# Optimization experiments

Hardware: AMD Instinct MI355X
Metric: run time of the kernel (lower is better)

The kernel has to match this reference:

```python
import math
import jax, jax.numpy as jnp
import numpy as np

B, L, D = 64, 1024, 64

def setup_inputs() -> dict:
    key = jax.random.key(0)
    k1, k2, k3, k4, k5, k6 = jax.random.split(key, 6)
    return {
        "queries": jax.random.normal(k1, (B, L, D), dtype=jnp.float32),
        "keys": jax.random.normal(k2, (B, L, D), dtype=jnp.float32),
        "values": jax.random.normal(k3, (B, L, D), dtype=jnp.float32),
        "pos_k": jax.random.normal(k4, (L, L, D), dtype=jnp.float32),
        "pos_v": jax.random.normal(k5, (L, L, D), dtype=jnp.float32),
        "valid_lens": jax.random.randint(k6, (B,), 0, L, dtype=jnp.int32),
    }

MASK_VALUE = -1e6  # matches torch source's -1000000.0 fill

def reference(queries, keys, values, pos_k, pos_v, valid_lens):
    d = queries.shape[-1]
    scale = 1.0 / math.sqrt(d)
    # content scores: [B, Lq, Lk]
    scores = jnp.einsum("bqd,bkd->bqk", queries, keys)
    # relative-position scores: contract each query position with its RPR key table
    scores_pos = jnp.einsum("bqd,qkd->bqk", queries, pos_k)
    scores = (scores + scores_pos) * scale
    # mask keys beyond valid_lens[b] with -1e6 (as in sequence_mask), then softmax
    kpos = jnp.arange(scores.shape[-1])
    mask = kpos[None, None, :] < valid_lens[:, None, None]  # [B,1,Lk] -> broadcast
    scores = jnp.where(mask, scores, MASK_VALUE)
    attn = jax.nn.softmax(scores, axis=-1)  # [B, Lq, Lk]
    # dropout prob = 0.0 -> identity
    out = jnp.einsum("bqk,bkd->bqd", attn, values)
    out_pos = jnp.einsum("bqk,qkd->bqd", attn, pos_v)
    return out + out_pos
```

## Files before the change

kernel.cpp:

```cpp
#include <hip/hip_runtime.h>
#include <hip/hip_bf16.h>

typedef __attribute__((ext_vector_type(8))) short bf16x8;
typedef __attribute__((ext_vector_type(4))) float f32x4;

#define B_SZ 64
#define L_SZ 1024
#define D_SZ 64
#define SCALE 0.125f

__device__ __forceinline__ short f2bf(float f) {
    union { float f; unsigned u; } v; v.f = f;
    unsigned r = (v.u + 0x7fffu + ((v.u >> 16) & 1u)) >> 16;
    return (short)r;
}

__device__ __forceinline__ bf16x8 cvt8(const float* __restrict__ p) {
    f32x4 a = *(const f32x4*)p;
    f32x4 b = *(const f32x4*)(p + 4);
    bf16x8 r;
    r[0] = f2bf(a[0]); r[1] = f2bf(a[1]); r[2] = f2bf(a[2]); r[3] = f2bf(a[3]);
    r[4] = f2bf(b[0]); r[5] = f2bf(b[1]); r[6] = f2bf(b[2]); r[7] = f2bf(b[3]);
    return r;
}

#define MFMA(A, Bf, C) __builtin_amdgcn_mfma_f32_16x16x32_bf16(A, Bf, C, 0, 0, 0)

__global__ void cvt_bf16_k(const float* __restrict__ src, short* __restrict__ dst, int n8) {
    const int stride = gridDim.x * blockDim.x;
    for (int i = blockIdx.x * blockDim.x + threadIdx.x; i < n8; i += stride) {
        *(bf16x8*)(dst + (size_t)i * 8) = cvt8(src + (size_t)i * 8);
    }
}

#define TP 72
__global__ void tr64_bf16_k(const float* __restrict__ src, short* __restrict__ dst) {
    __shared__ __attribute__((aligned(16))) short tile[64 * TP];
    const int kt = blockIdx.x;
    const size_t o = blockIdx.y;
    const int tid = threadIdx.x;
    {
        const int rr = tid >> 2, c0 = (tid & 3) << 4;
        const float* sp = src + (o * L_SZ + (size_t)(kt * 64 + rr)) * D_SZ + c0;
        *(bf16x8*)(tile + rr * TP + c0)     = cvt8(sp);
        *(bf16x8*)(tile + rr * TP + c0 + 8) = cvt8(sp + 8);
    }
    __syncthreads();
    {
        const int d = tid >> 2, k4 = (tid & 3) << 4;
        bf16x8 o0, o1;
#pragma unroll
        for (int j = 0; j < 8; ++j) {
            o0[j] = tile[(k4 + j) * TP + d];
            o1[j] = tile[(k4 + 8 + j) * TP + d];
        }
        short* dp = dst + (o * 64 + (size_t)d) * L_SZ + kt * 64 + k4;
        *(bf16x8*)dp       = o0;
        *(bf16x8*)(dp + 8) = o1;
    }
}

__global__ __launch_bounds__(512, 2) void rpr_attn_bf16(
    const short* __restrict__ Qb, const short* __restrict__ Kb,
    const short* __restrict__ Vt, const short* __restrict__ PKb,
    const short* __restrict__ PVt, const int* __restrict__ VLEN,
    float* __restrict__ OUT)
{
    __shared__ __attribute__((aligned(16))) float SA[2][256 * 32];
    __shared__ __attribute__((aligned(16))) short PB[2][256 * 64];

    const int tid = threadIdx.x;
    const int wave = tid >> 6, lane = tid & 63;
    const int g = wave >> 2, r = wave & 3;
    const int lane15 = lane & 15, quad = lane >> 4;

    const int n = blockIdx.x;
    const int l = (n & 7) * 32 + (n >> 3);
    const int b0 = (l & 3) * 16;
    const int q0 = (l >> 2) * 16;

    char* sa = (char*)&SA[g][0];
    char* pb = (char*)&PB[g][0];

    bf16x8 qa[4][2], qp[4][2];
    int vl[4];
#pragma unroll
    for (int j = 0; j < 4; ++j) {
        const int bl = r * 4 + j;
        vl[j] = VLEN[b0 + bl];
        const short* pc = Qb + ((b0 + bl) * L_SZ + q0 + lane15) * D_SZ + quad * 8;
        qa[j][0] = *(const bf16x8*)pc;
        qa[j][1] = *(const bf16x8*)(pc + 32);
        const short* pp = Qb + ((b0 + lane15) * L_SZ + q0 + bl) * D_SZ + quad * 8;
        qp[j][0] = *(const bf16x8*)pp;
        qp[j][1] = *(const bf16x8*)(pp + 32);
    }

    f32x4 Oc[4][4], Op[4][4];
    float es[4][4];
#pragma unroll
    for (int j = 0; j < 4; ++j)
#pragma unroll
        for (int nt = 0; nt < 4; ++nt) {
            Oc[j][nt] = (f32x4){0.f, 0.f, 0.f, 0.f};
            Op[j][nt] = (f32x4){0.f, 0.f, 0.f, 0.f};
            es[j][nt] = 0.f;
        }

    for (int it = 0; it < 16; ++it) {
        const int kb = g * 512 + it * 32;

#pragma unroll
        for (int j = 0; j < 4; ++j) {
            const int ql = r * 4 + j;
#pragma unroll
            for (int c = 0; c < 2; ++c) {
                const short* bp = PKb + ((q0 + ql) * L_SZ + kb + c * 16 + lane15) * D_SZ + quad * 8;
                f32x4 acc = (f32x4){0.f, 0.f, 0.f, 0.f};
                acc = MFMA(qp[j][0], *(const bf16x8*)bp, acc);
                acc = MFMA(qp[j][1], *(const bf16x8*)(bp + 32), acc);
#pragma unroll
                for (int i = 0; i < 4; ++i) {
                    const int brow = quad * 4 + i;
                    const int off = (((brow * 16 + ql) * 32 + c * 16 + lane15) * 4)
                                    ^ (((brow ^ ql) & 7) << 4);
                    *(float*)(sa + off) = acc[i];
                }
            }
        }
        __syncthreads();

#pragma unroll
        for (int j = 0; j < 4; ++j) {
            const int bl = r * 4 + j;
#pragma unroll
            for (int c = 0; c < 2; ++c) {
                const short* bp = Kb + ((b0 + bl) * L_SZ + kb + c * 16 + lane15) * D_SZ + quad * 8;
                f32x4 acc = (f32x4){0.f, 0.f, 0.f, 0.f};
                acc = MFMA(qa[j][0], *(const bf16x8*)bp, acc);
                acc = MFMA(qa[j][1], *(const bf16x8*)(bp + 32), acc);
                const int kg = kb + c * 16 + lane15;
#pragma unroll
                for (int i = 0; i < 4; ++i) {
                    const int q = quad * 4 + i;
                    const int soff = (((bl * 16 + q) * 32 + c * 16 + lane15) * 4)
                                     ^ (((bl ^ q) & 7) << 4);
                    const float s = (acc[i] + *(const float*)(sa + soff)) * SCALE;
                    float e;
                    if (vl[j] == 0)       e = 1.0f;
                    else if (kg < vl[j])  e = __expf(s);
                    else                  e = 0.0f;
                    es[j][i] += e;
                    const int poff = (((bl * 16 + q) * 64 + c * 16 + lane15) * 2)
                                     ^ (((bl ^ q) & 7) << 4);
                    *(short*)(pb + poff) = f2bf(e);
                }
            }
        }
        __syncthreads();

#pragma unroll
        for (int j = 0; j < 4; ++j) {
            const int bl = r * 4 + j;
            const int aoff = (((bl * 16 + lane15) * 64) * 2 + quad * 16)
                             ^ (((bl ^ lane15) & 7) << 4);
            const bf16x8 af = *(const bf16x8*)(pb + aoff);
            const short* vb = Vt + ((b0 + bl) * 64 + lane15) * L_SZ + kb + quad * 8;
#pragma unroll
            for (int nt = 0; nt < 4; ++nt) {
                const bf16x8 bf = *(const bf16x8*)(vb + nt * 16 * L_SZ);
                Oc[j][nt] = MFMA(af, bf, Oc[j][nt]);
            }
        }
#pragma unroll
        for (int j = 0; j < 4; ++j) {
            const int ql = r * 4 + j;
            const int aoff = (((lane15 * 16 + ql) * 64) * 2 + quad * 16)
                             ^ (((lane15 ^ ql) & 7) << 4);
            const bf16x8 af = *(const bf16x8*)(pb + aoff);
            const short* vb = PVt + ((q0 + ql) * 64 + lane15) * L_SZ + kb + quad * 8;
#pragma unroll
            for (int nt = 0; nt < 4; ++nt) {
                const bf16x8 bf = *(const bf16x8*)(vb + nt * 16 * L_SZ);
                Op[j][nt] = MFMA(af, bf, Op[j][nt]);
            }
        }
        __syncthreads();
    }

    float* lball = (float*)&PB[0][0];
#pragma unroll
    for (int j = 0; j < 4; ++j)
#pragma unroll
        for (int i = 0; i < 4; ++i) {
            float s = es[j][i];
            s += __shfl_xor(s, 1);
            s += __shfl_xor(s, 2);
            s += __shfl_xor(s, 4);
            s += __shfl_xor(s, 8);
            if (lane15 == 0)
                lball[g * 256 + (r * 4 + j) * 16 + quad * 4 + i] = s;
        }

    float* Obuf = &SA[0][0];

    if (g == 0) {
#pragma unroll
        for (int j = 0; j < 4; ++j)
#pragma unroll
            for (int nt = 0; nt < 4; ++nt)
#pragma unroll
                for (int i = 0; i < 4; ++i)
                    Obuf[((r * 4 + j) * 16 + quad * 4 + i) * 64 + nt * 16 + lane15] = Oc[j][nt][i];
    }
    __syncthreads();
    if (g == 1) {
#pragma unroll
        for (int j = 0; j < 4; ++j)
#pragma unroll
            for (int nt = 0; nt < 4; ++nt)
#pragma unroll
                for (int i = 0; i < 4; ++i)
                    Obuf[((r * 4 + j) * 16 + quad * 4 + i) * 64 + nt * 16 + lane15] += Oc[j][nt][i];
    }
    __syncthreads();
    if (g == 0) {
#pragma unroll
        for (int j = 0; j < 4; ++j)
#pragma unroll
            for (int nt = 0; nt < 4; ++nt)
#pragma unroll
                for (int i = 0; i < 4; ++i)
                    Obuf[((quad * 4 + i) * 16 + r * 4 + j) * 64 + nt * 16 + lane15] += Op[j][nt][i];
    }
    __syncthreads();
    if (g == 1) {
#pragma unroll
        for (int j = 0; j < 4; ++j)
#pragma unroll
            for (int nt = 0; nt < 4; ++nt)
#pragma unroll
                for (int i = 0; i < 4; ++i)
                    Obuf[((quad * 4 + i) * 16 + r * 4 + j) * 64 + nt * 16 + lane15] += Op[j][nt][i];
    }
    __syncthreads();

    for (int idx = tid; idx < 4096; idx += 512) {
        const int d4 = idx & 15, ql2 = (idx >> 4) & 15, bl2 = idx >> 8;
        const float li = lball[bl2 * 16 + ql2] + lball[256 + bl2 * 16 + ql2];
        const float rl = 1.0f / li;
        f32x4 o = *(const f32x4*)&Obuf[(bl2 * 16 + ql2) * 64 + d4 * 4];
        o[0] *= rl; o[1] *= rl; o[2] *= rl; o[3] *= rl;
        *(f32x4*)&OUT[((b0 + bl2) * L_SZ + q0 + ql2) * D_SZ + d4 * 4] = o;
    }
}

#define KP 36
#define BPITCH 580
#define SA_SZ 9280

__global__ __launch_bounds__(512, 2) void rpr_attn(
    const float* __restrict__ Q, const float* __restrict__ Kt,
    const float* __restrict__ V, const float* __restrict__ PK,
    const float* __restrict__ PV, const int* __restrict__ VLEN,
    float* __restrict__ OUT)
{
    __shared__ float SA[2][SA_SZ];
    __shared__ float lbuf[2][256];

    const int tid = threadIdx.x;
    const int wave = tid >> 6, lane = tid & 63;
    const int g = wave >> 2, r = wave & 3;
    const int lane15 = lane & 15, quad = lane >> 4;
    const int b0 = blockIdx.x * 16;
    const int q0 = blockIdx.y * 16;

    float* sa = SA[g];

    bf16x8 qa[4][2], qp[4][2];
    int vl[4];
#pragma unroll
    for (int j = 0; j < 4; ++j) {
        const int bl = r * 4 + j;
        vl[j] = VLEN[b0 + bl];
        const float* pc = Q + ((b0 + bl) * L_SZ + q0 + lane15) * D_SZ + quad * 8;
        qa[j][0] = cvt8(pc); qa[j][1] = cvt8(pc + 32);
        const float* pp = Q + ((b0 + lane15) * L_SZ + q0 + bl) * D_SZ + quad * 8;
        qp[j][0] = cvt8(pp); qp[j][1] = cvt8(pp + 32);
    }

    f32x4 Oc[4][4], Op[4][4];
#pragma unroll
    for (int j = 0; j < 4; ++j)
#pragma unroll
        for (int nt = 0; nt < 4; ++nt) {
            Oc[j][nt] = (f32x4){0.f, 0.f, 0.f, 0.f};
            Op[j][nt] = (f32x4){0.f, 0.f, 0.f, 0.f};
        }
    float l_acc = 0.f;

    const int tg = r * 64 + lane;
    const int lb = tg >> 4, lq = tg & 15;

    for (int it = 0; it < 16; ++it) {
        const int kb = g * 512 + it * 32;

#pragma unroll
        for (int j = 0; j < 4; ++j) {
            const int ql = r * 4 + j;
#pragma unroll
            for (int c = 0; c < 2; ++c) {
                const float* bp = PK + ((q0 + ql) * L_SZ + kb + c * 16 + lane15) * D_SZ + quad * 8;
                f32x4 acc = (f32x4){0.f, 0.f, 0.f, 0.f};
                acc = MFMA(qp[j][0], cvt8(bp), acc);
                acc = MFMA(qp[j][1], cvt8(bp + 32), acc);
#pragma unroll
                for (int i = 0; i < 4; ++i)
                    sa[(quad * 4 + i) * BPITCH + ql * KP + c * 16 + lane15] = acc[i];
            }
        }
        __syncthreads();

#pragma unroll
        for (int j = 0; j < 4; ++j) {
            const int bl = r * 4 + j;
#pragma unroll
            for (int c = 0; c < 2; ++c) {
                const float* bp = Kt + ((b0 + bl) * L_SZ + kb + c * 16 + lane15) * D_SZ + quad * 8;
                f32x4 acc = (f32x4){0.f, 0.f, 0.f, 0.f};
                acc = MFMA(qa[j][0], cvt8(bp), acc);
                acc = MFMA(qa[j][1], cvt8(bp + 32), acc);
                const int kg = kb + c * 16 + lane15;
#pragma unroll
                for (int i = 0; i < 4; ++i) {
                    const int idx = bl * BPITCH + (quad * 4 + i) * KP + c * 16 + lane15;
                    const float s = (acc[i] + sa[idx]) * SCALE;
                    float e;
                    if (vl[j] == 0)       e = 1.0f;
                    else if (kg < vl[j])  e = __expf(s);
                    else                  e = 0.0f;
                    sa[idx] = e;
                }
            }
        }
        __syncthreads();

        {
            const float* row = sa + lb * BPITCH + lq * KP;
            float s = 0.f;
#pragma unroll
            for (int kk = 0; kk < 32; kk += 4) {
                f32x4 v4 = *(const f32x4*)(row + kk);
                s += v4[0] + v4[1] + v4[2] + v4[3];
            }
            l_acc += s;
        }
#pragma unroll
        for (int j = 0; j < 4; ++j) {
            const int bl = r * 4 + j;
            const bf16x8 af = cvt8(sa + bl * BPITCH + lane15 * KP + quad * 8);
            const float* vb = V + ((b0 + bl) * L_SZ + kb + quad * 8) * D_SZ + lane15;
#pragma unroll
            for (int nt = 0; nt < 4; ++nt) {
                bf16x8 bf;
#pragma unroll
                for (int jj = 0; jj < 8; ++jj) bf[jj] = f2bf(vb[jj * D_SZ + nt * 16]);
                Oc[j][nt] = MFMA(af, bf, Oc[j][nt]);
            }
        }
#pragma unroll
        for (int j = 0; j < 4; ++j) {
            const int ql = r * 4 + j;
            const bf16x8 af = cvt8(sa + lane15 * BPITCH + ql * KP + quad * 8);
            const float* vb = PV + ((q0 + ql) * L_SZ + kb + quad * 8) * D_SZ + lane15;
#pragma unroll
            for (int nt = 0; nt < 4; ++nt) {
                bf16x8 bf;
#pragma unroll
                for (int jj = 0; jj < 8; ++jj) bf[jj] = f2bf(vb[jj * D_SZ + nt * 16]);
                Op[j][nt] = MFMA(af, bf, Op[j][nt]);
            }
        }
        __syncthreads();
    }

    lbuf[g][tg] = l_acc;
    float* Obuf = &SA[0][0];

    if (g == 0) {
#pragma unroll
        for (int j = 0; j < 4; ++j)
#pragma unroll
            for (int nt = 0; nt < 4; ++nt)
#pragma unroll
                for (int i = 0; i < 4; ++i)
                    Obuf[((r * 4 + j) * 16 + quad * 4 + i) * 64 + nt * 16 + lane15] = Oc[j][nt][i];
    }
    __syncthreads();
    if (g == 1) {
#pragma unroll
        for (int j = 0; j < 4; ++j)
#pragma unroll
            for (int nt = 0; nt < 4; ++nt)
#pragma unroll
                for (int i = 0; i < 4; ++i)
                    Obuf[((r * 4 + j) * 16 + quad * 4 + i) * 64 + nt * 16 + lane15] += Oc[j][nt][i];
    }
    __syncthreads();
    if (g == 0) {
#pragma unroll
        for (int j = 0; j < 4; ++j)
#pragma unroll
            for (int nt = 0; nt < 4; ++nt)
#pragma unroll
                for (int i = 0; i < 4; ++i)
                    Obuf[((quad * 4 + i) * 16 + r * 4 + j) * 64 + nt * 16 + lane15] += Op[j][nt][i];
    }
    __syncthreads();
    if (g == 1) {
#pragma unroll
        for (int j = 0; j < 4; ++j)
#pragma unroll
            for (int nt = 0; nt < 4; ++nt)
#pragma unroll
                for (int i = 0; i < 4; ++i)
                    Obuf[((quad * 4 + i) * 16 + r * 4 + j) * 64 + nt * 16 + lane15] += Op[j][nt][i];
    }
    __syncthreads();

    for (int idx = tid; idx < 4096; idx += 512) {
        const int d4 = idx & 15, ql2 = (idx >> 4) & 15, bl2 = idx >> 8;
        const float li = lbuf[0][bl2 * 16 + ql2] + lbuf[1][bl2 * 16 + ql2];
        const float rl = 1.0f / li;
        f32x4 o = *(const f32x4*)&Obuf[(bl2 * 16 + ql2) * 64 + d4 * 4];
        o[0] *= rl; o[1] *= rl; o[2] *= rl; o[3] *= rl;
        *(f32x4*)&OUT[((b0 + bl2) * L_SZ + q0 + ql2) * D_SZ + d4 * 4] = o;
    }
}

extern "C" void kernel_launch(void* const* d_in, const int* in_sizes, int n_in,
                              void* d_out, int out_size, void* d_ws, size_t ws_size,
                              hipStream_t stream) {
    (void)in_sizes; (void)n_in; (void)out_size;
    const float* Q  = (const float*)d_in[0];
    const float* K  = (const float*)d_in[1];
    const float* V  = (const float*)d_in[2];
    const float* PK = (const float*)d_in[3];
    const float* PV = (const float*)d_in[4];
    const int*   VL = (const int*)d_in[5];
    float* OUT = (float*)d_out;

    const size_t WS_NEEDED = (3ull * 4194304ull + 2ull * 67108864ull) * 2ull;

    if (d_ws != nullptr && ws_size >= WS_NEEDED) {
        short* Qb  = (short*)d_ws;
        short* Kb  = Qb + 4194304;
        short* Vt  = Kb + 4194304;
        short* PKb = Vt + 4194304;
        short* PVt = PKb + 67108864;

        cvt_bf16_k<<<dim3(1024), dim3(256), 0, stream>>>(Q, Qb, 524288);
        cvt_bf16_k<<<dim3(1024), dim3(256), 0, stream>>>(K, Kb, 524288);
        cvt_bf16_k<<<dim3(2048), dim3(256), 0, stream>>>(PK, PKb, 8388608);
        tr64_bf16_k<<<dim3(16, 64),   dim3(256), 0, stream>>>(V, Vt);
        tr64_bf16_k<<<dim3(16, 1024), dim3(256), 0, stream>>>(PV, PVt);

        rpr_attn_bf16<<<dim3(256), dim3(512), 0, stream>>>(Qb, Kb, Vt, PKb, PVt, VL, OUT);
    } else {
        dim3 grid(4, 64, 1);
        dim3 block(512, 1, 1);
        rpr_attn<<<grid, block, 0, stream>>>(Q, K, V, PK, PV, VL, OUT);
    }
}
```

Baseline: 1.259 ms.

## Drop bf16 pre-conversion of Q/K/PK, split key range across blocks with merge kernel

Removes the separate fp32→bf16 conversion kernels for Q, K and PK and converts them in registers inside the attention kernel. This avoids writing and re-reading a large bf16 copy of PK. The two key halves now run in separate 256-thread blocks that write partial outputs and row sums to workspace, and a new merge kernel combines them and normalizes. The change also adds s_setprio around the PV MFMA phase, drops a per-iteration barrier, and reworks the transpose kernel to stage fp32 in a padded tile. The cost is reading PK at fp32 width inside the main kernel plus an extra partial-output round trip through global memory.

```diff
diff --git a/kernel.cpp b/kernel.cpp
--- a/kernel.cpp
+++ b/kernel.cpp
@@ -4,7 +4,6 @@
 typedef __attribute__((ext_vector_type(8))) short bf16x8;
 typedef __attribute__((ext_vector_type(4))) float f32x4;
 
-#define B_SZ 64
 #define L_SZ 1024
 #define D_SZ 64
 #define SCALE 0.125f
@@ -26,24 +25,23 @@
 
 #define MFMA(A, Bf, C) __builtin_amdgcn_mfma_f32_16x16x32_bf16(A, Bf, C, 0, 0, 0)
 
-__global__ void cvt_bf16_k(const float* __restrict__ src, short* __restrict__ dst, int n8) {
-    const int stride = gridDim.x * blockDim.x;
-    for (int i = blockIdx.x * blockDim.x + threadIdx.x; i < n8; i += stride) {
-        *(bf16x8*)(dst + (size_t)i * 8) = cvt8(src + (size_t)i * 8);
-    }
-}
-
-#define TP 72
 __global__ void tr64_bf16_k(const float* __restrict__ src, short* __restrict__ dst) {
-    __shared__ __attribute__((aligned(16))) short tile[64 * TP];
+    __shared__ float tile[64 * 65];
     const int kt = blockIdx.x;
     const size_t o = blockIdx.y;
     const int tid = threadIdx.x;
     {
         const int rr = tid >> 2, c0 = (tid & 3) << 4;
         const float* sp = src + (o * L_SZ + (size_t)(kt * 64 + rr)) * D_SZ + c0;
-        *(bf16x8*)(tile + rr * TP + c0)     = cvt8(sp);
-        *(bf16x8*)(tile + rr * TP + c0 + 8) = cvt8(sp + 8);
+        f32x4 v0 = *(const f32x4*)sp;
+        f32x4 v1 = *(const f32x4*)(sp + 4);
+        f32x4 v2 = *(const f32x4*)(sp + 8);
+        f32x4 v3 = *(const f32x4*)(sp + 12);
+        float* tp = tile + rr * 65 + c0;
+        tp[0] = v0[0];  tp[1] = v0[1];  tp[2] = v0[2];  tp[3] = v0[3];
+        tp[4] = v1[0];  tp[5] = v1[1];  tp[6] = v1[2];  tp[7] = v1[3];
+        tp[8] = v2[0];  tp[9] = v2[1];  tp[10] = v2[2]; tp[11] = v2[3];
+        tp[12] = v3[0]; tp[13] = v3[1]; tp[14] = v3[2]; tp[15] = v3[3];
     }
     __syncthreads();
     {
@@ -51,8 +49,8 @@
         bf16x8 o0, o1;
 #pragma unroll
         for (int j = 0; j < 8; ++j) {
-            o0[j] = tile[(k4 + j) * TP + d];
-            o1[j] = tile[(k4 + 8 + j) * TP + d];
+            o0[j] = f2bf(tile[(k4 + j) * 65 + d]);
+            o1[j] = f2bf(tile[(k4 + 8 + j) * 65 + d]);
         }
         short* dp = dst + (o * 64 + (size_t)d) * L_SZ + kt * 64 + k4;
         *(bf16x8*)dp       = o0;
@@ -60,27 +58,27 @@
     }
 }
 
-__global__ __launch_bounds__(512, 2) void rpr_attn_bf16(
-    const short* __restrict__ Qb, const short* __restrict__ Kb,
-    const short* __restrict__ Vt, const short* __restrict__ PKb,
-    const short* __restrict__ PVt, const int* __restrict__ VLEN,
-    float* __restrict__ OUT)
+__global__ __launch_bounds__(256, 2) void rpr_attn2(
+    const float* __restrict__ Q, const float* __restrict__ K,
+    const float* __restrict__ PK,
+    const short* __restrict__ Vt, const short* __restrict__ PVt,
+    const int* __restrict__ VLEN,
+    float* __restrict__ Opart, float* __restrict__ Lp)
 {
-    __shared__ __attribute__((aligned(16))) float SA[2][256 * 32];
-    __shared__ __attribute__((aligned(16))) short PB[2][256 * 64];
+    __shared__ __attribute__((aligned(16))) float SH[16384 + 256];
+    char* sa = (char*)&SH[0];
+    char* pb = (char*)&SH[8192];
+    float* lbuf = &SH[16384];
 
     const int tid = threadIdx.x;
-    const int wave = tid >> 6, lane = tid & 63;
-    const int g = wave >> 2, r = wave & 3;
+    const int r = tid >> 6, lane = tid & 63;
     const int lane15 = lane & 15, quad = lane >> 4;
 
     const int n = blockIdx.x;
-    const int l = (n & 7) * 32 + (n >> 3);
+    const int l = (n & 7) * 64 + (n >> 3);
     const int b0 = (l & 3) * 16;
-    const int q0 = (l >> 2) * 16;
-
-    char* sa = (char*)&SA[g][0];
-    char* pb = (char*)&PB[g][0];
+    const int ks = (l >> 2) & 1;
+    const int q0 = (l >> 3) * 16;
 
     bf16x8 qa[4][2], qp[4][2];
     int vl[4];
@@ -88,12 +86,10 @@
     for (int j = 0; j < 4; ++j) {
         const int bl = r * 4 + j;
         vl[j] = VLEN[b0 + bl];
-        const short* pc = Qb + ((b0 + bl) * L_SZ + q0 + lane15) * D_SZ + quad * 8;
-        qa[j][0] = *(const bf16x8*)pc;
-        qa[j][1] = *(const bf16x8*)(pc + 32);
-        const short* pp = Qb + ((b0 + lane15) * L_SZ + q0 + bl) * D_SZ + quad * 8;
-        qp[j][0] = *(const bf16x8*)pp;
-        qp[j][1] = *(const bf16x8*)(pp + 32);
+        const float* pc = Q + ((b0 + bl) * L_SZ + q0 + lane15) * D_SZ + quad * 8;
+        qa[j][0] = cvt8(pc); qa[j][1] = cvt8(pc + 32);
+        const float* pp = Q + ((b0 + lane15) * L_SZ + q0 + bl) * D_SZ + quad * 8;
+        qp[j][0] = cvt8(pp); qp[j][1] = cvt8(pp + 32);
     }
 
     f32x4 Oc[4][4], Op[4][4];
@@ -108,17 +104,17 @@
         }
 
     for (int it = 0; it < 16; ++it) {
-        const int kb = g * 512 + it * 32;
+        const int kb = ks * 512 + it * 32;
 
 #pragma unroll
         for (int j = 0; j < 4; ++j) {
             const int ql = r * 4 + j;
 #pragma unroll
             for (int c = 0; c < 2; ++c) {
-                const short* bp = PKb + ((q0 + ql) * L_SZ + kb + c * 16 + lane15) * D_SZ + quad * 8;
+                const float* bp = PK + ((q0 + ql) * L_SZ + kb + c * 16 + lane15) * D_SZ + quad * 8;
                 f32x4 acc = (f32x4){0.f, 0.f, 0.f, 0.f};
-                acc = MFMA(qp[j][0], *(const bf16x8*)bp, acc);
-                acc = MFMA(qp[j][1], *(const bf16x8*)(bp + 32), acc);
+                acc = MFMA(qp[j][0], cvt8(bp), acc);
+                acc = MFMA(qp[j][1], cvt8(bp + 32), acc);
 #pragma unroll
                 for (int i = 0; i < 4; ++i) {
                     const int brow = quad * 4 + i;
@@ -135,10 +131,10 @@
             const int bl = r * 4 + j;
 #pragma unroll
             for (int c = 0; c < 2; ++c) {
-                const short* bp = Kb + ((b0 + bl) * L_SZ + kb + c * 16 + lane15) * D_SZ + quad * 8;
+                const float* bp = K + ((b0 + bl) * L_SZ + kb + c * 16 + lane15) * D_SZ + quad * 8;
                 f32x4 acc = (f32x4){0.f, 0.f, 0.f, 0.f};
-                acc = MFMA(qa[j][0], *(const bf16x8*)bp, acc);
-                acc = MFMA(qa[j][1], *(const bf16x8*)(bp + 32), acc);
+                acc = MFMA(qa[j][0], cvt8(bp), acc);
+                acc = MFMA(qa[j][1], cvt8(bp + 32), acc);
                 const int kg = kb + c * 16 + lane15;
 #pragma unroll
                 for (int i = 0; i < 4; ++i) {
@@ -159,6 +155,7 @@
         }
         __syncthreads();
 
+        __builtin_amdgcn_s_setprio(1);
 #pragma unroll
         for (int j = 0; j < 4; ++j) {
             const int bl = r * 4 + j;
@@ -185,10 +182,9 @@
                 Op[j][nt] = MFMA(af, bf, Op[j][nt]);
             }
         }
-        __syncthreads();
-    }
-
-    float* lball = (float*)&PB[0][0];
+        __builtin_amdgcn_s_setprio(0);
+    }
+
 #pragma unroll
     for (int j = 0; j < 4; ++j)
 #pragma unroll
@@ -199,59 +195,55 @@
             s += __shfl_xor(s, 4);
             s += __shfl_xor(s, 8);
             if (lane15 == 0)
-                lball[g * 256 + (r * 4 + j) * 16 + quad * 4 + i] = s;
-        }
-
-    float* Obuf = &SA[0][0];
-
-    if (g == 0) {
-#pragma unroll
-        for (int j = 0; j < 4; ++j)
-#pragma unroll
-            for (int nt = 0; nt < 4; ++nt)
-#pragma unroll
-                for (int i = 0; i < 4; ++i)
-                    Obuf[((r * 4 + j) * 16 + quad * 4 + i) * 64 + nt * 16 + lane15] = Oc[j][nt][i];
-    }
-    __syncthreads();
-    if (g == 1) {
-#pragma unroll
-        for (int j = 0; j < 4; ++j)
-#pragma unroll
-            for (int nt = 0; nt < 4; ++nt)
-#pragma unroll
-                for (int i = 0; i < 4; ++i)
-                    Obuf[((r * 4 + j) * 16 + quad * 4 + i) * 64 + nt * 16 + lane15] += Oc[j][nt][i];
-    }
-    __syncthreads();
-    if (g == 0) {
-#pragma unroll
-        for (int j = 0; j < 4; ++j)
-#pragma unroll
-            for (int nt = 0; nt < 4; ++nt)
-#pragma unroll
-                for (int i = 0; i < 4; ++i)
-                    Obuf[((quad * 4 + i) * 16 + r * 4 + j) * 64 + nt * 16 + lane15] += Op[j][nt][i];
-    }
-    __syncthreads();
-    if (g == 1) {
-#pragma unroll
-        for (int j = 0; j < 4; ++j)
-#pragma unroll
-            for (int nt = 0; nt < 4; ++nt)
-#pragma unroll
-                for (int i = 0; i < 4; ++i)
-                    Obuf[((quad * 4 + i) * 16 + r * 4 + j) * 64 + nt * 16 + lane15] += Op[j][nt][i];
-    }
-    __syncthreads();
-
-    for (int idx = tid; idx < 4096; idx += 512) {
+                lbuf[(r * 4 + j) * 16 + quad * 4 + i] = s;
+        }
+    __syncthreads();
+
+    float* Obuf = &SH[0];
+
+#pragma unroll
+    for (int j = 0; j < 4; ++j)
+#pragma unroll
+        for (int nt = 0; nt < 4; ++nt)
+#pragma unroll
+            for (int i = 0; i < 4; ++i)
+                Obuf[((r * 4 + j) * 16 + quad * 4 + i) * 64 + nt * 16 + lane15] = Oc[j][nt][i];
+    __syncthreads();
+#pragma unroll
+    for (int j = 0; j < 4; ++j)
+#pragma unroll
+        for (int nt = 0; nt < 4; ++nt)
+#pragma unroll
+            for (int i = 0; i < 4; ++i)
+                Obuf[((quad * 4 + i) * 16 + r * 4 + j) * 64 + nt * 16 + lane15] += Op[j][nt][i];
+    __syncthreads();
+
+    const size_t obase = (size_t)ks * 4194304;
+    for (int idx = tid; idx < 4096; idx += 256) {
         const int d4 = idx & 15, ql2 = (idx >> 4) & 15, bl2 = idx >> 8;
-        const float li = lball[bl2 * 16 + ql2] + lball[256 + bl2 * 16 + ql2];
-        const float rl = 1.0f / li;
         f32x4 o = *(const f32x4*)&Obuf[(bl2 * 16 + ql2) * 64 + d4 * 4];
-        o[0] *= rl; o[1] *= rl; o[2] *= rl; o[3] *= rl;
-        *(f32x4*)&OUT[((b0 + bl2) * L_SZ + q0 + ql2) * D_SZ + d4 * 4] = o;
+        *(f32x4*)&Opart[obase + (((size_t)(b0 + bl2) * L_SZ) + q0 + ql2) * D_SZ + d4 * 4] = o;
+    }
+    {
+        const int ql2 = tid & 15, bl2 = tid >> 4;
+        Lp[ks * 65536 + (b0 + bl2) * L_SZ + q0 + ql2] = lbuf[bl2 * 16 + ql2];
+    }
+}
+
+__global__ void merge_k(const float* __restrict__ Opart, const float* __restrict__ Lp,
+                        float* __restrict__ OUT) {
+    const int stride = gridDim.x * blockDim.x;
+    for (int u = blockIdx.x * blockDim.x + threadIdx.x; u < 1048576; u += stride) {
+        const int bq = u >> 4;
+        const float rl = 1.0f / (Lp[bq] + Lp[65536 + bq]);
+        f32x4 a = *(const f32x4*)(Opart + (size_t)u * 4);
+        f32x4 b = *(const f32x4*)(Opart + 4194304ull + (size_t)u * 4);
+        f32x4 o;
+        o[0] = (a[0] + b[0]) * rl;
+        o[1] = (a[1] + b[1]) * rl;
+        o[2] = (a[2] + b[2]) * rl;
+        o[3] = (a[3] + b[3]) * rl;
+        *(f32x4*)(OUT + (size_t)u * 4) = o;
     }
 }
 
@@ -450,22 +442,18 @@
     const int*   VL = (const int*)d_in[5];
     float* OUT = (float*)d_out;
 
-    const size_t WS_NEEDED = (3ull * 4194304ull + 2ull * 67108864ull) * 2ull;
+    const size_t WS_NEEDED = 8388608ull + 134217728ull + 33554432ull + 524288ull;
 
     if (d_ws != nullptr && ws_size >= WS_NEEDED) {
-        short* Qb  = (short*)d_ws;
-        short* Kb  = Qb + 4194304;
-        short* Vt  = Kb + 4194304;
-        short* PKb = Vt + 4194304;
-        short* PVt = PKb + 67108864;
-
-        cvt_bf16_k<<<dim3(1024), dim3(256), 0, stream>>>(Q, Qb, 524288);
-        cvt_bf16_k<<<dim3(1024), dim3(256), 0, stream>>>(K, Kb, 524288);
-        cvt_bf16_k<<<dim3(2048), dim3(256), 0, stream>>>(PK, PKb, 8388608);
+        short* Vt    = (short*)d_ws;
+        short* PVt   = Vt + 4194304;
+        float* Opart = (float*)(PVt + 67108864);
+        float* Lp    = Opart + 8388608;
+
         tr64_bf16_k<<<dim3(16, 64),   dim3(256), 0, stream>>>(V, Vt);
         tr64_bf16_k<<<dim3(16, 1024), dim3(256), 0, stream>>>(PV, PVt);
-
-        rpr_attn_bf16<<<dim3(256), dim3(512), 0, stream>>>(Qb, Kb, Vt, PKb, PVt, VL, OUT);
+        rpr_attn2<<<dim3(512), dim3(256), 0, stream>>>(Q, K, PK, Vt, PVt, VL, Opart, Lp);
+        merge_k<<<dim3(2048), dim3(256), 0, stream>>>(Opart, Lp, OUT);
     } else {
         dim3 grid(4, 64, 1);
         dim3 block(512, 1, 1);
```

Result: slower. 1.442 ms (+14.5%).
